# Kernel optimization log

Hardware: AMD Instinct MI355X
Metric: run time of the kernel (lower is better)

## Reference

```python
import jax, jax.numpy as jnp
from jax import lax
import numpy as np

B, L, E, D, A, M, V, T = 64, 196, 2048, 512, 512, 512, 30000, 21


def setup_inputs() -> dict:
    key = jax.random.key(0)
    ks = jax.random.split(key, 22)
    s = 0.02
    encoder_out = jax.random.normal(ks[0], (B, L, E), jnp.float32)
    captions = jax.random.randint(ks[1], (B, T), 0, V, dtype=jnp.int32)
    lens = jax.random.randint(ks[2], (B,), 2, T + 1, dtype=jnp.int32)
    caption_lengths = jnp.sort(lens)[::-1]  # descending, as torch loop requires
    p = {
        'W_enc': jax.random.normal(ks[3], (E, A)) * s, 'b_enc': jnp.zeros((A,)),
        'W_dec': jax.random.normal(ks[4], (D, A)) * s, 'b_dec': jnp.zeros((A,)),
        'w_att': jax.random.normal(ks[5], (A, 1)) * s, 'b_att': jnp.zeros((1,)),
        'emb': jax.random.uniform(ks[6], (V, M), minval=-0.1, maxval=0.1),
        'W_ih': jax.random.normal(ks[7], (M + E, 4 * D)) * s, 'b_ih': jnp.zeros((4 * D,)),
        'W_hh': jax.random.normal(ks[8], (D, 4 * D)) * s, 'b_hh': jnp.zeros((4 * D,)),
        'W_h0': jax.random.normal(ks[9], (E, D)) * s, 'b_h0': jnp.zeros((D,)),
        'W_c0': jax.random.normal(ks[10], (E, D)) * s, 'b_c0': jnp.zeros((D,)),
        'W_beta': jax.random.normal(ks[11], (D, E)) * s, 'b_beta': jnp.zeros((E,)),
        'W_fc': jax.random.uniform(ks[12], (D, V), minval=-0.1, maxval=0.1), 'b_fc': jnp.zeros((V,)),
    }
    return {'encoder_out': encoder_out, 'captions': captions,
            'caption_lengths': caption_lengths, **p}


def reference(encoder_out, captions, caption_lengths,
              W_enc, b_enc, W_dec, b_dec, w_att, b_att, emb,
              W_ih, b_ih, W_hh, b_hh, W_h0, b_h0, W_c0, b_c0,
              W_beta, b_beta, W_fc, b_fc):
    max_len = captions.shape[1] - 1  # teacher forcing: predict y_1..y_T
    x_emb = emb[captions]            # [B,T,M]  (dropout = identity in eval)

    mean_enc = encoder_out.mean(axis=1)
    h0 = jnp.tanh(mean_enc @ W_h0 + b_h0)
    c0 = jnp.tanh(mean_enc @ W_c0 + b_c0)

    # enc projection is constant across timesteps -> hoist out of the loop
    e_proj = encoder_out @ W_enc + b_enc  # [B,L,A]

    # mask[b,t] = (caption_lengths[b]-1) > t  (valid only because lens sorted desc,
    # matching the torch batch_t truncation exactly)
    mask = (caption_lengths[:, None] - 1) > jnp.arange(max_len)[None, :]

    def step(carry, xs):
        h, c = carry
        emb_t, m = xs  # [B,M], [B]
        d = h @ W_dec + b_dec                                   # [B,A]
        energy = (jax.nn.relu(e_proj + d[:, None, :]) @ w_att)[..., 0] + b_att[0]  # [B,L]
        alpha = jax.nn.softmax(energy, axis=1)
        ctx = jnp.einsum('ble,bl->be', encoder_out, alpha)      # [B,E]
        gate = jax.nn.sigmoid(h @ W_beta + b_beta)
        x = jnp.concatenate([emb_t, gate * ctx], axis=1)        # [B,M+E]
        gates = x @ W_ih + b_ih + h @ W_hh + b_hh               # [B,4D]
        i, f, g, o = jnp.split(gates, 4, axis=1)
        c_new = jax.nn.sigmoid(f) * c + jax.nn.sigmoid(i) * jnp.tanh(g)
        h_new = jax.nn.sigmoid(o) * jnp.tanh(c_new)
        pred = h_new @ W_fc + b_fc                              # [B,V]
        mf = m[:, None].astype(pred.dtype)
        return (h_new, c_new), (pred * mf, alpha * mf)

    xs = (jnp.swapaxes(x_emb[:, :max_len, :], 0, 1), mask.T)    # time-major
    _, (preds, alphas) = lax.scan(step, (h0, c0), xs)
    predictions = jnp.swapaxes(preds, 0, 1)                     # [B,max_len,V]
    alphas = jnp.swapaxes(alphas, 0, 1)                         # [B,max_len,L]
    return predictions, alphas
```

## Files before the change

kernel.cpp:

```cpp
#include <hip/hip_runtime.h>
#include <math.h>

namespace {

constexpr int NB  = 64;
constexpr int NL  = 196;
constexpr int NE  = 2048;
constexpr int ND  = 512;
constexpr int NA  = 512;
constexpr int NM  = 512;
constexpr int NV  = 30000;
constexpr int NT  = 21;
constexpr int NML = 20;
constexpr int NG  = 4 * ND;
constexpr int KXG = NM + NE;
constexpr int KSPL = 8, KSL = KXG / KSPL;
constexpr int NDG = ND + NE + NG;
constexpr int OFF_GATE = ND;
constexpr int OFF_HWHH = ND + NE;

constexpr size_t WS_MEAN = 0;
constexpr size_t WS_C0   = WS_MEAN + (size_t)NB * NE;
constexpr size_t WS_C1   = WS_C0   + (size_t)NB * ND;
constexpr size_t WS_D    = WS_C1   + (size_t)NB * ND;
constexpr size_t WS_GATE = WS_D    + (size_t)NB * NA;
constexpr size_t WS_HWHH = WS_GATE + (size_t)NB * NE;
constexpr size_t WS_EN   = WS_HWHH + (size_t)NB * NG;
constexpr size_t WS_PP   = WS_EN   + (size_t)NB * NL;
constexpr size_t WS_SHB  = WS_PP   + (size_t)1048576;
constexpr size_t SH_HALL = 0;
constexpr size_t SH_XEMB = SH_HALL + (size_t)(NML + 1) * NB * ND;
constexpr size_t SH_GCTX = SH_XEMB + (size_t)NML * NB * NM;
constexpr size_t SH_EPROJ= SH_GCTX + (size_t)NB * NE;
constexpr size_t SH_WET  = SH_EPROJ+ (size_t)NB * NL * NA;
constexpr size_t SH_WIHX = SH_WET  + (size_t)NA * NE;
constexpr size_t SH_WALL = SH_WIHX + (size_t)NG * KXG;
constexpr size_t SH_WFC  = SH_WALL + (size_t)NDG * ND;
constexpr size_t SH_ENCBF= SH_WFC  + (size_t)NV * ND;
constexpr size_t SH_END  = SH_ENCBF+ (size_t)NB * NL * NE;
constexpr size_t BYTES_ENC = WS_SHB * 4 + SH_END * 2;

typedef __attribute__((ext_vector_type(8))) short short8v;
typedef __attribute__((ext_vector_type(4))) float f32x4;

__device__ __forceinline__ float sigmoidf_(float x) { return 1.f / (1.f + expf(-x)); }
__device__ __forceinline__ short f2bf(float f) {
  unsigned u = __float_as_uint(f);
  return (short)((u + 0x7FFFu + ((u >> 16) & 1u)) >> 16);
}
__device__ __forceinline__ float bf2f(short s) {
  return __uint_as_float(((unsigned)(unsigned short)s) << 16);
}


__device__ __forceinline__ void gload16(const short* g, short* l) {
  __builtin_amdgcn_global_load_lds(
      (const __attribute__((address_space(1))) unsigned int*)(g),
      (__attribute__((address_space(3))) unsigned int*)(l), 16, 0, 0);
}

template <int R>
__device__ __forceinline__ void stage_direct(const short* __restrict__ src, int ldK,
                                             int rowClamp, short* lds, int tid) {
  int wv = tid >> 6, lane = tid & 63;
  int sub = lane >> 3;
  int kb  = (lane & 7) ^ sub;
#pragma unroll
  for (int g = wv; g < R / 8; g += 4) {
    int row = g * 8 + sub;
    int r = row < rowClamp ? row : rowClamp;
    gload16(src + (size_t)r * ldK + (kb << 3), lds + g * 512);
  }
}

template <int R>
__device__ __forceinline__ void stage_f32cvt(const float* __restrict__ src, int ldK,
                                             short* lds, int tid) {
#pragma unroll
  for (int cidx = tid; cidx < R * 8; cidx += 256) {
    int row = cidx >> 3, kb = cidx & 7;
    const float* p = src + (size_t)row * ldK + kb * 8;
    float4 x = *(const float4*)p;
    float4 y = *(const float4*)(p + 4);
    short8v s;
    s[0] = f2bf(x.x); s[1] = f2bf(x.y); s[2] = f2bf(x.z); s[3] = f2bf(x.w);
    s[4] = f2bf(y.x); s[5] = f2bf(y.y); s[6] = f2bf(y.z); s[7] = f2bf(y.w);
    *(short8v*)(lds + row * 64 + ((kb ^ (row & 7)) << 3)) = s;
  }
}

template <int FM, int FN>
__device__ __forceinline__ void mma_tiles(const short* ldsA, const short* ldsB,
                                          int wr, int wc, int lane, f32x4 acc[FM][FN]) {
  int l15 = lane & 15;
#pragma unroll
  for (int kk = 0; kk < 2; ++kk) {
    int kb0 = kk * 4 + (lane >> 4);
    short8v a[FM], b[FN];
#pragma unroll
    for (int m = 0; m < FM; ++m) {
      int row = wr * FM * 16 + m * 16 + l15;
      a[m] = *(const short8v*)(ldsA + row * 64 + ((kb0 ^ (row & 7)) << 3));
    }
#pragma unroll
    for (int n = 0; n < FN; ++n) {
      int row = wc * FN * 16 + n * 16 + l15;
      b[n] = *(const short8v*)(ldsB + row * 64 + ((kb0 ^ (row & 7)) << 3));
    }
#pragma unroll
    for (int m = 0; m < FM; ++m)
#pragma unroll
      for (int n = 0; n < FN; ++n)
        acc[m][n] = __builtin_amdgcn_mfma_f32_16x16x32_bf16(a[m], b[n], acc[m][n], 0, 0, 0);
  }
}


template <bool PERM>
__global__ __launch_bounds__(256) void k_tcvt(const float* __restrict__ src, int Ks, int Ns,
                                              short* __restrict__ dst, int ldDst, int kOff) {
  __shared__ float tbuf[32][33];
  int n0 = blockIdx.x * 32, k0 = blockIdx.y * 32;
  int tx = threadIdx.x, ty = threadIdx.y;
#pragma unroll
  for (int i = 0; i < 32; i += 8) {
    int k = k0 + ty + i, n = n0 + tx;
    tbuf[ty + i][tx] = (k < Ks && n < Ns) ? src[(size_t)k * Ns + n] : 0.f;
  }
  __syncthreads();
#pragma unroll
  for (int i = 0; i < 32; i += 8) {
    int n = n0 + ty + i, k = k0 + tx;
    if (n < Ns && k < Ks) {
      int nd = PERM ? (((n & 511) << 2) | (n >> 9)) : n;
      dst[(size_t)nd * ldDst + kOff + k] = f2bf(tbuf[tx][ty + i]);
    }
  }
}

template <bool BF>
__global__ __launch_bounds__(256) void k_prep(const float* __restrict__ enc,
                                              short* __restrict__ encbf,
                                              float* __restrict__ mean_enc) {
  int b = blockIdx.y;
  int e = blockIdx.x * 256 + threadIdx.x;
  const float* p = enc + (size_t)b * NL * NE + e;
  short* q = encbf + (size_t)b * NL * NE + e;
  float s = 0.f;
  for (int l = 0; l < NL; ++l) {
    float v = p[(size_t)l * NE];
    s += v;
    if (BF) q[(size_t)l * NE] = f2bf(v);
  }
  mean_enc[(size_t)b * NE + e] = s * (1.f / NL);
}

__global__ void k_xemb(const int* __restrict__ caps, const float* __restrict__ emb,
                       short* __restrict__ xemb) {
  int i = blockIdx.x * 256 + threadIdx.x;
  int m = i & (NM - 1), b = (i >> 9) & (NB - 1), t = i >> 15;
  xemb[i] = f2bf(emb[(size_t)caps[b * NT + t] * NM + m]);
}

__global__ void k_init0(const float* __restrict__ mean_enc, const float* __restrict__ W_h0,
                        const float* __restrict__ W_c0, float* __restrict__ PP) {
  int idx = blockIdx.x * 256 + threadIdx.x;
  int ks = blockIdx.y;
  int b = idx >> 10, jh = idx & 1023, half = jh >> 9, j = jh & 511;
  const float* W = half ? W_c0 : W_h0;
  const float* mp = mean_enc + (size_t)b * NE + ks * 128;
  const float* Wp = W + (size_t)(ks * 128) * ND + j;
  float acc = 0.f;
#pragma unroll 4
  for (int k = 0; k < 128; ++k) acc = fmaf(mp[k], Wp[(size_t)k * ND], acc);
  PP[(size_t)ks * 65536 + idx] = acc;
}

__global__ void k_init1(const float* __restrict__ PP, const float* __restrict__ b_h0,
                        const float* __restrict__ b_c0, float* __restrict__ c0,
                        short* __restrict__ h0) {
  int idx = blockIdx.x * 256 + threadIdx.x;
  int b = idx >> 9, j = idx & 511;
  float ah = b_h0[j], ac = b_c0[j];
  for (int s = 0; s < 16; ++s) {
    const float* p = PP + (size_t)s * 65536 + b * 1024;
    ah += p[j]; ac += p[512 + j];
  }
  c0[idx] = tanhf(ac);
  h0[idx] = f2bf(tanhf(ah));
}

template <bool BF>
__global__ __launch_bounds__(256) void k_eproj(const float* __restrict__ enc,
                                               const short* __restrict__ encbf,
                                               const short* __restrict__ We_t,
                                               const float* __restrict__ b_enc,
                                               short* __restrict__ e_proj) {
  constexpr int FM = 4, FN = 4;
  __shared__ short ldsA[128 * 64], ldsB[128 * 64];
  int p = blockIdx.x;
  int l = (p & 7) * 49 + (p >> 3);
  int bn = (l & 3) * 128, bm = (l >> 2) * 128;
  int tid = threadIdx.x, lane = tid & 63, wave = tid >> 6, wr = wave >> 1, wc = wave & 1;
  f32x4 acc[FM][FN];
#pragma unroll
  for (int m = 0; m < FM; ++m)
#pragma unroll
    for (int n = 0; n < FN; ++n) acc[m][n] = (f32x4){0.f, 0.f, 0.f, 0.f};
  for (int k0 = 0; k0 < NE; k0 += 64) {
    __syncthreads();
    if (BF) stage_direct<128>(encbf + (size_t)bm * NE + k0, NE, 127, ldsA, tid);
    else    stage_f32cvt<128>(enc + (size_t)bm * NE + k0, NE, ldsA, tid);
    stage_direct<128>(We_t + (size_t)bn * NE + k0, NE, 127, ldsB, tid);
    __syncthreads();
    mma_tiles<FM, FN>(ldsA, ldsB, wr, wc, lane, acc);
  }
#pragma unroll
  for (int m = 0; m < FM; ++m)
#pragma unroll
    for (int n = 0; n < FN; ++n) {
      int col = bn + wc * FN * 16 + n * 16 + (lane & 15);
      float bias = b_enc[col];
#pragma unroll
      for (int r = 0; r < 4; ++r) {
        int row = bm + wr * FM * 16 + m * 16 + (lane >> 4) * 4 + r;
        e_proj[(size_t)row * NA + col] = f2bf(acc[m][n][r] + bias);
      }
    }
}

__global__ __launch_bounds__(256) void k_hgemm_dg(const short* __restrict__ h_bf,
                                                  const short* __restrict__ Wall_t,
                                                  const float* __restrict__ b_dec,
                                                  const float* __restrict__ b_beta,
                                                  float* __restrict__ d_buf,
                                                  float* __restrict__ gatebuf,
                                                  float* __restrict__ hWhh) {
  constexpr int FM = 2, FN = 2;
  __shared__ short ldsA[64 * 64], ldsB[64 * 64];
  int bn = blockIdx.x * 64;
  int tid = threadIdx.x, lane = tid & 63, wave = tid >> 6, wr = wave >> 1, wc = wave & 1;
  f32x4 acc[FM][FN];
#pragma unroll
  for (int m = 0; m < FM; ++m)
#pragma unroll
    for (int n = 0; n < FN; ++n) acc[m][n] = (f32x4){0.f, 0.f, 0.f, 0.f};
  for (int k0 = 0; k0 < ND; k0 += 64) {
    __syncthreads();
    stage_direct<64>(h_bf + k0, ND, 63, ldsA, tid);
    stage_direct<64>(Wall_t + (size_t)bn * ND + k0, ND, 63, ldsB, tid);
    __syncthreads();
    mma_tiles<FM, FN>(ldsA, ldsB, wr, wc, lane, acc);
  }
#pragma unroll
  for (int m = 0; m < FM; ++m)
#pragma unroll
    for (int r = 0; r < 4; ++r) {
      int row = wr * FM * 16 + m * 16 + (lane >> 4) * 4 + r;
#pragma unroll
      for (int n = 0; n < FN; ++n) {
        int col = bn + wc * FN * 16 + n * 16 + (lane & 15);
        float a = acc[m][n][r];
        if (bn < OFF_GATE) {
          d_buf[(size_t)row * NA + col] = a + b_dec[col];
        } else if (bn < OFF_HWHH) {
          int e = col - OFF_GATE;
          gatebuf[(size_t)row * NE + e] = sigmoidf_(a + b_beta[e]);
        } else {
          hWhh[(size_t)row * NG + (col - OFF_HWHH)] = a;
        }
      }
    }
}


__global__ __launch_bounds__(256) void k_energy(const short* __restrict__ e_proj,
                                                const float* __restrict__ d_buf,
                                                const float* __restrict__ w_att,
                                                const float* __restrict__ b_att,
                                                float* __restrict__ energy) {
  int tid = threadIdx.x, wave = tid >> 6, lane = tid & 63;
  int row = blockIdx.x * 4 + wave;
  int b = row / NL;
  short8v ev = *(const short8v*)(e_proj + (size_t)row * NA + lane * 8);
  const float* dp = d_buf + (size_t)b * NA + lane * 8;
  float4 d0 = *(const float4*)dp, d1 = *(const float4*)(dp + 4);
  const float* wp = w_att + lane * 8;
  float4 w0 = *(const float4*)wp, w1 = *(const float4*)(wp + 4);
  float dd[8] = {d0.x, d0.y, d0.z, d0.w, d1.x, d1.y, d1.z, d1.w};
  float ww[8] = {w0.x, w0.y, w0.z, w0.w, w1.x, w1.y, w1.z, w1.w};
  float acc = 0.f;
#pragma unroll
  for (int i = 0; i < 8; ++i) {
    float v = bf2f(ev[i]) + dd[i];
    acc = fmaf(fmaxf(v, 0.f), ww[i], acc);
  }
#pragma unroll
  for (int off = 32; off; off >>= 1) acc += __shfl_down(acc, off);
  if (lane == 0) energy[row] = acc + b_att[0];
}

template <bool BF>
__global__ __launch_bounds__(256) void k_ctx(const short* __restrict__ encbf,
                                             const float* __restrict__ encf,
                                             const float* __restrict__ energy,
                                             const float* __restrict__ gatebuf,
                                             const int* __restrict__ clen,
                                             short* __restrict__ gctx,
                                             float* __restrict__ alphas_out, int t) {
  int b = blockIdx.y, e0 = blockIdx.x * 512, tid = threadIdx.x;
  __shared__ float al[NL];
  __shared__ float red[8];
  int wave = tid >> 6, lane = tid & 63;
  float v = (tid < NL) ? energy[b * NL + tid] : -INFINITY;
  float mx = v;
#pragma unroll
  for (int off = 32; off; off >>= 1) mx = fmaxf(mx, __shfl_down(mx, off));
  if (lane == 0) red[wave] = mx;
  __syncthreads();
  if (tid == 0) red[0] = fmaxf(fmaxf(red[0], red[1]), fmaxf(red[2], red[3]));
  __syncthreads();
  mx = red[0];
  float ex = (tid < NL) ? expf(v - mx) : 0.f;
  float sm = ex;
#pragma unroll
  for (int off = 32; off; off >>= 1) sm += __shfl_down(sm, off);
  if (lane == 0) red[4 + wave] = sm;
  __syncthreads();
  if (tid == 0) red[0] = 1.f / (red[4] + red[5] + red[6] + red[7]);
  __syncthreads();
  float alv = ex * red[0];
  if (tid < NL) {
    al[tid] = alv;
    if (blockIdx.x == 0) {
      float mf = ((clen[b] - 1) > t) ? 1.f : 0.f;
      alphas_out[((size_t)b * NML + t) * NL + tid] = alv * mf;
    }
  }
  __syncthreads();
  float cx0 = 0.f, cx1 = 0.f;
  if (BF) {
    const unsigned* p = (const unsigned*)(encbf + (size_t)b * NL * NE + e0) + tid;
#pragma unroll 4
    for (int l = 0; l < NL; ++l) {
      unsigned u = p[(size_t)l * (NE / 2)];
      cx0 = fmaf(al[l], bf2f((short)(u & 0xffffu)), cx0);
      cx1 = fmaf(al[l], bf2f((short)(u >> 16)), cx1);
    }
  } else {
    const float* p = encf + (size_t)b * NL * NE + e0 + 2 * tid;
#pragma unroll 4
    for (int l = 0; l < NL; ++l) {
      float2 u = *(const float2*)(p + (size_t)l * NE);
      cx0 = fmaf(al[l], u.x, cx0);
      cx1 = fmaf(al[l], u.y, cx1);
    }
  }
  int e = e0 + 2 * tid;
  const float* gp = gatebuf + (size_t)b * NE + e;
  unsigned out = (unsigned)(unsigned short)f2bf(cx0 * gp[0]) |
                 ((unsigned)(unsigned short)f2bf(cx1 * gp[1]) << 16);
  *(unsigned*)(gctx + (size_t)b * NE + e) = out;
}

__global__ __launch_bounds__(256) void k_gates(const short* __restrict__ xemb_t,
                                               const short* __restrict__ gctx,
                                               const short* __restrict__ Wihx_t,
                                               float* __restrict__ P) {
  constexpr int FM = 2, FN = 2;
  __shared__ short ldsA[64 * 64], ldsB[64 * 64];
  int bn = blockIdx.x * 64, ks = blockIdx.y;
  int tid = threadIdx.x, lane = tid & 63, wave = tid >> 6, wr = wave >> 1, wc = wave & 1;
  f32x4 acc[FM][FN];
#pragma unroll
  for (int m = 0; m < FM; ++m)
#pragma unroll
    for (int n = 0; n < FN; ++n) acc[m][n] = (f32x4){0.f, 0.f, 0.f, 0.f};
  int kend = (ks + 1) * KSL;
  for (int k0 = ks * KSL; k0 < kend; k0 += 64) {
    const short* asrc; int aldk;
    if (k0 < NM) { asrc = xemb_t + k0;      aldk = NM; }
    else         { asrc = gctx + (k0 - NM); aldk = NE; }
    __syncthreads();
    stage_direct<64>(asrc, aldk, 63, ldsA, tid);
    stage_direct<64>(Wihx_t + (size_t)bn * KXG + k0, KXG, 63, ldsB, tid);
    __syncthreads();
    mma_tiles<FM, FN>(ldsA, ldsB, wr, wc, lane, acc);
  }
#pragma unroll
  for (int m = 0; m < FM; ++m)
#pragma unroll
    for (int n = 0; n < FN; ++n) {
      int col = bn + wc * FN * 16 + n * 16 + (lane & 15);
#pragma unroll
      for (int r = 0; r < 4; ++r) {
        int row = wr * FM * 16 + m * 16 + (lane >> 4) * 4 + r;
        P[((size_t)ks * NB + row) * NG + col] = acc[m][n][r];
      }
    }
}

__global__ void k_lstm(const float* __restrict__ P, const float* __restrict__ hWhh,
                       const float* __restrict__ b_ih, const float* __restrict__ b_hh,
                       const float* __restrict__ c_prev, float* __restrict__ c_next,
                       short* __restrict__ h_next) {
  int idx = blockIdx.x * 256 + threadIdx.x;
  int b = idx >> 9, j = idx & (ND - 1);
  float4 hw = *(const float4*)&hWhh[(size_t)b * NG + j * 4];
  float gi = b_ih[j] + b_hh[j] + hw.x;
  float gf = b_ih[j + ND] + b_hh[j + ND] + hw.y;
  float gg = b_ih[j + 2 * ND] + b_hh[j + 2 * ND] + hw.z;
  float go = b_ih[j + 3 * ND] + b_hh[j + 3 * ND] + hw.w;
#pragma unroll
  for (int s = 0; s < KSPL; ++s) {
    float4 v = *(const float4*)&P[((size_t)s * NB + b) * NG + j * 4];
    gi += v.x; gf += v.y; gg += v.z; go += v.w;
  }
  float cn = sigmoidf_(gf) * c_prev[idx] + sigmoidf_(gi) * tanhf(gg);
  float hn = sigmoidf_(go) * tanhf(cn);
  c_next[idx] = cn;
  h_next[idx] = f2bf(hn);
}

__global__ __launch_bounds__(256) void k_pred(const short* __restrict__ h_all1,
                                              const short* __restrict__ Wfc_t,
                                              const float* __restrict__ b_fc,
                                              const int* __restrict__ clen,
                                              float* __restrict__ preds) {
  constexpr int FM = 4, FN = 4;
  constexpr int NT_M = 10, NT_N = (NV + 127) / 128;
  constexpr int TOT = NT_M * NT_N;
  __shared__ short ldsA[128 * 64], ldsB[128 * 64];
  int p = blockIdx.x;
  int q = TOT / 8, r8 = TOT % 8;
  int xcd = p & 7, i = p >> 3;
  int l = (xcd < r8 ? xcd * (q + 1) : r8 * (q + 1) + (xcd - r8) * q) + i;
  int bm = (l % NT_M) * 128, bn = (l / NT_M) * 128;
  int tid = threadIdx.x, lane = tid & 63, wave = tid >> 6, wr = wave >> 1, wc = wave & 1;
  int rowClampB = NV - 1 - bn; if (rowClampB > 127) rowClampB = 127;
  f32x4 acc[FM][FN];
#pragma unroll
  for (int m = 0; m < FM; ++m)
#pragma unroll
    for (int n = 0; n < FN; ++n) acc[m][n] = (f32x4){0.f, 0.f, 0.f, 0.f};
  for (int k0 = 0; k0 < ND; k0 += 64) {
    __syncthreads();
    stage_direct<128>(h_all1 + (size_t)bm * ND + k0, ND, 127, ldsA, tid);
    stage_direct<128>(Wfc_t + (size_t)bn * ND + k0, ND, rowClampB, ldsB, tid);
    __syncthreads();
    mma_tiles<FM, FN>(ldsA, ldsB, wr, wc, lane, acc);
  }
#pragma unroll
  for (int m = 0; m < FM; ++m)
#pragma unroll
    for (int n = 0; n < FN; ++n) {
      int col = bn + wc * FN * 16 + n * 16 + (lane & 15);
      if (col < NV) {
        float bias = b_fc[col];
#pragma unroll
        for (int r = 0; r < 4; ++r) {
          int row = bm + wr * FM * 16 + m * 16 + (lane >> 4) * 4 + r;
          int t = row >> 6, b = row & 63;
          float mf = ((clen[b] - 1) > t) ? 1.f : 0.f;
          preds[((size_t)b * NML + t) * NV + col] = mf * (acc[m][n][r] + bias);
        }
      }
    }
}

}

extern "C" void kernel_launch(void* const* d_in, const int* in_sizes, int n_in,
                              void* d_out, int out_size, void* d_ws, size_t ws_size,
                              hipStream_t stream) {
  (void)in_sizes; (void)n_in; (void)out_size;
  const float* enc    = (const float*)d_in[0];
  const int*   caps   = (const int*)d_in[1];
  const int*   clen   = (const int*)d_in[2];
  const float* W_enc  = (const float*)d_in[3];
  const float* b_enc  = (const float*)d_in[4];
  const float* W_dec  = (const float*)d_in[5];
  const float* b_dec  = (const float*)d_in[6];
  const float* w_att  = (const float*)d_in[7];
  const float* b_att  = (const float*)d_in[8];
  const float* emb    = (const float*)d_in[9];
  const float* W_ih   = (const float*)d_in[10];
  const float* b_ih   = (const float*)d_in[11];
  const float* W_hh   = (const float*)d_in[12];
  const float* b_hh   = (const float*)d_in[13];
  const float* W_h0   = (const float*)d_in[14];
  const float* b_h0   = (const float*)d_in[15];
  const float* W_c0   = (const float*)d_in[16];
  const float* b_c0   = (const float*)d_in[17];
  const float* W_beta = (const float*)d_in[18];
  const float* b_beta = (const float*)d_in[19];
  const float* W_fc   = (const float*)d_in[20];
  const float* b_fc   = (const float*)d_in[21];

  float* ws     = (float*)d_ws;
  float* preds  = (float*)d_out;
  float* alphas = preds + (size_t)NB * NML * NV;

  float* mean_enc = ws + WS_MEAN;
  float* cbuf[2]  = {ws + WS_C0, ws + WS_C1};
  float* d_buf    = ws + WS_D;
  float* gatebuf  = ws + WS_GATE;
  float* hWhh     = ws + WS_HWHH;
  float* energy   = ws + WS_EN;
  float* PP       = ws + WS_PP;
  short* shb      = (short*)(ws + WS_SHB);
  short* h_all    = shb + SH_HALL;
  short* xemb     = shb + SH_XEMB;
  short* gctx     = shb + SH_GCTX;
  short* e_proj   = shb + SH_EPROJ;
  short* We_t     = shb + SH_WET;
  short* Wihx_t   = shb + SH_WIHX;
  short* Wall_t   = shb + SH_WALL;
  short* Wfc_t    = shb + SH_WFC;
  short* encbf    = shb + SH_ENCBF;
  const bool use_bf = ws_size >= BYTES_ENC;

  k_tcvt<false><<<dim3(NA / 32, NE / 32), dim3(32, 8), 0, stream>>>(W_enc, NE, NA, We_t, NE, 0);
  k_tcvt<true><<<dim3(NG / 32, KXG / 32), dim3(32, 8), 0, stream>>>(
      W_ih, KXG, NG, Wihx_t, KXG, 0);
  k_tcvt<false><<<dim3(NA / 32, ND / 32), dim3(32, 8), 0, stream>>>(W_dec, ND, NA, Wall_t, ND, 0);
  k_tcvt<false><<<dim3(NE / 32, ND / 32), dim3(32, 8), 0, stream>>>(
      W_beta, ND, NE, Wall_t + (size_t)OFF_GATE * ND, ND, 0);
  k_tcvt<true><<<dim3(NG / 32, ND / 32), dim3(32, 8), 0, stream>>>(
      W_hh, ND, NG, Wall_t + (size_t)OFF_HWHH * ND, ND, 0);
  k_tcvt<false><<<dim3((NV + 31) / 32, ND / 32), dim3(32, 8), 0, stream>>>(
      W_fc, ND, NV, Wfc_t, ND, 0);
  if (use_bf)
    k_prep<true><<<dim3(NE / 256, NB), 256, 0, stream>>>(enc, encbf, mean_enc);
  else
    k_prep<false><<<dim3(NE / 256, NB), 256, 0, stream>>>(enc, encbf, mean_enc);
  k_xemb<<<(NML * NB * NM) / 256, 256, 0, stream>>>(caps, emb, xemb);

  k_init0<<<dim3(256, 16), 256, 0, stream>>>(mean_enc, W_h0, W_c0, PP);
  k_init1<<<(NB * ND) / 256, 256, 0, stream>>>(PP, b_h0, b_c0, cbuf[0], h_all);
  if (use_bf)
    k_eproj<true><<<392, 256, 0, stream>>>(enc, encbf, We_t, b_enc, e_proj);
  else
    k_eproj<false><<<392, 256, 0, stream>>>(enc, encbf, We_t, b_enc, e_proj);
  k_hgemm_dg<<<NDG / 64, 256, 0, stream>>>(h_all, Wall_t, b_dec, b_beta,
                                           d_buf, gatebuf, hWhh);

  for (int t = 0; t < NML; ++t) {
    short* h_next = h_all + (size_t)(t + 1) * NB * ND;
    float* c_prev = cbuf[t & 1];
    float* c_next = cbuf[1 - (t & 1)];
    k_energy<<<(NB * NL) / 4, 256, 0, stream>>>(e_proj, d_buf, w_att, b_att, energy);
    if (use_bf)
      k_ctx<true><<<dim3(NE / 512, NB), 256, 0, stream>>>(encbf, enc, energy, gatebuf,
                                                          clen, gctx, alphas, t);
    else
      k_ctx<false><<<dim3(NE / 512, NB), 256, 0, stream>>>(encbf, enc, energy, gatebuf,
                                                           clen, gctx, alphas, t);
    k_gates<<<dim3(NG / 64, KSPL), 256, 0, stream>>>(xemb + (size_t)t * NB * NM, gctx,
                                                     Wihx_t, PP);
    k_lstm<<<(NB * ND) / 256, 256, 0, stream>>>(PP, hWhh, b_ih, b_hh, c_prev, c_next,
                                                h_next);
    if (t + 1 < NML)
      k_hgemm_dg<<<NDG / 64, 256, 0, stream>>>(h_next, Wall_t, b_dec, b_beta,
                                               d_buf, gatebuf, hWhh);
  }
  k_pred<<<10 * ((NV + 127) / 128), 256, 0, stream>>>(h_all + (size_t)NB * ND, Wfc_t,
                                                      b_fc, clen, preds);
}
```

Baseline: 1.173 ms.

## Fuse attention energy into context kernel and stage prediction stores through LDS

Removes the separate per-step energy kernel. Each context block now computes its batch row's 196 attention energies into shared memory before the softmax, which drops 20 launches and the global round trip for the energies. Because the grid has four E-chunk blocks per batch row, the energy work is done four times over. The prediction GEMM epilogue now writes its accumulators to padded LDS and stores coalesced float4 rows, replacing scattered scalar stores into the large prediction output.

```diff
diff --git a/kernel.cpp b/kernel.cpp
--- a/kernel.cpp
+++ b/kernel.cpp
@@ -274,45 +274,43 @@
 }
 
 
-__global__ __launch_bounds__(256) void k_energy(const short* __restrict__ e_proj,
-                                                const float* __restrict__ d_buf,
-                                                const float* __restrict__ w_att,
-                                                const float* __restrict__ b_att,
-                                                float* __restrict__ energy) {
-  int tid = threadIdx.x, wave = tid >> 6, lane = tid & 63;
-  int row = blockIdx.x * 4 + wave;
-  int b = row / NL;
-  short8v ev = *(const short8v*)(e_proj + (size_t)row * NA + lane * 8);
-  const float* dp = d_buf + (size_t)b * NA + lane * 8;
-  float4 d0 = *(const float4*)dp, d1 = *(const float4*)(dp + 4);
-  const float* wp = w_att + lane * 8;
-  float4 w0 = *(const float4*)wp, w1 = *(const float4*)(wp + 4);
-  float dd[8] = {d0.x, d0.y, d0.z, d0.w, d1.x, d1.y, d1.z, d1.w};
-  float ww[8] = {w0.x, w0.y, w0.z, w0.w, w1.x, w1.y, w1.z, w1.w};
-  float acc = 0.f;
-#pragma unroll
-  for (int i = 0; i < 8; ++i) {
-    float v = bf2f(ev[i]) + dd[i];
-    acc = fmaf(fmaxf(v, 0.f), ww[i], acc);
-  }
-#pragma unroll
-  for (int off = 32; off; off >>= 1) acc += __shfl_down(acc, off);
-  if (lane == 0) energy[row] = acc + b_att[0];
-}
-
 template <bool BF>
-__global__ __launch_bounds__(256) void k_ctx(const short* __restrict__ encbf,
-                                             const float* __restrict__ encf,
-                                             const float* __restrict__ energy,
-                                             const float* __restrict__ gatebuf,
-                                             const int* __restrict__ clen,
-                                             short* __restrict__ gctx,
-                                             float* __restrict__ alphas_out, int t) {
+__global__ __launch_bounds__(256) void k_actx(const short* __restrict__ e_proj,
+                                              const float* __restrict__ d_buf,
+                                              const float* __restrict__ w_att,
+                                              const float* __restrict__ b_att,
+                                              const short* __restrict__ encbf,
+                                              const float* __restrict__ encf,
+                                              const float* __restrict__ gatebuf,
+                                              const int* __restrict__ clen,
+                                              short* __restrict__ gctx,
+                                              float* __restrict__ alphas_out, int t) {
   int b = blockIdx.y, e0 = blockIdx.x * 512, tid = threadIdx.x;
+  __shared__ float e_sh[NL];
   __shared__ float al[NL];
   __shared__ float red[8];
   int wave = tid >> 6, lane = tid & 63;
-  float v = (tid < NL) ? energy[b * NL + tid] : -INFINITY;
+  const float* dp = d_buf + (size_t)b * NA + lane * 8;
+  float4 d0v = *(const float4*)dp, d1v = *(const float4*)(dp + 4);
+  const float* wp = w_att + lane * 8;
+  float4 w0v = *(const float4*)wp, w1v = *(const float4*)(wp + 4);
+  float dd[8] = {d0v.x, d0v.y, d0v.z, d0v.w, d1v.x, d1v.y, d1v.z, d1v.w};
+  float ww[8] = {w0v.x, w0v.y, w0v.z, w0v.w, w1v.x, w1v.y, w1v.z, w1v.w};
+  float batt = b_att[0];
+  for (int l = wave; l < NL; l += 4) {
+    short8v ev = *(const short8v*)(e_proj + (size_t)(b * NL + l) * NA + lane * 8);
+    float acc = 0.f;
+#pragma unroll
+    for (int i = 0; i < 8; ++i) {
+      float v = bf2f(ev[i]) + dd[i];
+      acc = fmaf(fmaxf(v, 0.f), ww[i], acc);
+    }
+#pragma unroll
+    for (int off = 32; off; off >>= 1) acc += __shfl_down(acc, off);
+    if (lane == 0) e_sh[l] = acc + batt;
+  }
+  __syncthreads();
+  float v = (tid < NL) ? e_sh[tid] : -INFINITY;
   float mx = v;
 #pragma unroll
   for (int off = 32; off; off >>= 1) mx = fmaxf(mx, __shfl_down(mx, off));
@@ -430,7 +428,10 @@
   constexpr int FM = 4, FN = 4;
   constexpr int NT_M = 10, NT_N = (NV + 127) / 128;
   constexpr int TOT = NT_M * NT_N;
-  __shared__ short ldsA[128 * 64], ldsB[128 * 64];
+  __shared__ __align__(16) char smem[64 * 129 * 4];
+  short* ldsA = (short*)smem;
+  short* ldsB = ldsA + 128 * 64;
+  float* fl   = (float*)smem;
   int p = blockIdx.x;
   int q = TOT / 8, r8 = TOT % 8;
   int xcd = p & 7, i = p >> 3;
@@ -450,22 +451,44 @@
     __syncthreads();
     mma_tiles<FM, FN>(ldsA, ldsB, wr, wc, lane, acc);
   }
-#pragma unroll
-  for (int m = 0; m < FM; ++m)
-#pragma unroll
-    for (int n = 0; n < FN; ++n) {
-      int col = bn + wc * FN * 16 + n * 16 + (lane & 15);
-      if (col < NV) {
-        float bias = b_fc[col];
-#pragma unroll
-        for (int r = 0; r < 4; ++r) {
-          int row = bm + wr * FM * 16 + m * 16 + (lane >> 4) * 4 + r;
-          int t = row >> 6, b = row & 63;
-          float mf = ((clen[b] - 1) > t) ? 1.f : 0.f;
-          preds[((size_t)b * NML + t) * NV + col] = mf * (acc[m][n][r] + bias);
+  __syncthreads();
+#pragma unroll
+  for (int h = 0; h < 2; ++h) {
+    if (wr == h) {
+#pragma unroll
+      for (int m = 0; m < FM; ++m)
+#pragma unroll
+        for (int n = 0; n < FN; ++n)
+#pragma unroll
+          for (int r = 0; r < 4; ++r) {
+            int lr = m * 16 + (lane >> 4) * 4 + r;
+            int lc = wc * 64 + n * 16 + (lane & 15);
+            fl[lr * 129 + lc] = acc[m][n][r];
+          }
+    }
+    __syncthreads();
+    {
+      int lr = tid & 63, cs = (tid >> 6) * 32;
+      int grow = bm + h * 64 + lr;
+      int tt = grow >> 6, bb = grow & 63;
+      float mf = ((clen[bb] - 1) > tt) ? 1.f : 0.f;
+      size_t obase = ((size_t)bb * NML + tt) * NV + bn + cs;
+#pragma unroll
+      for (int j = 0; j < 8; ++j) {
+        int col = bn + cs + j * 4;
+        if (col < NV) {
+          const float* fp = &fl[lr * 129 + cs + j * 4];
+          float4 v;
+          v.x = mf * (fp[0] + b_fc[col]);
+          v.y = mf * (fp[1] + b_fc[col + 1]);
+          v.z = mf * (fp[2] + b_fc[col + 2]);
+          v.w = mf * (fp[3] + b_fc[col + 3]);
+          *(float4*)(preds + obase + j * 4) = v;
         }
       }
     }
+    __syncthreads();
+  }
 }
 
 }
@@ -506,7 +529,6 @@
   float* d_buf    = ws + WS_D;
   float* gatebuf  = ws + WS_GATE;
   float* hWhh     = ws + WS_HWHH;
-  float* energy   = ws + WS_EN;
   float* PP       = ws + WS_PP;
   short* shb      = (short*)(ws + WS_SHB);
   short* h_all    = shb + SH_HALL;
@@ -549,13 +571,14 @@
     short* h_next = h_all + (size_t)(t + 1) * NB * ND;
     float* c_prev = cbuf[t & 1];
     float* c_next = cbuf[1 - (t & 1)];
-    k_energy<<<(NB * NL) / 4, 256, 0, stream>>>(e_proj, d_buf, w_att, b_att, energy);
     if (use_bf)
-      k_ctx<true><<<dim3(NE / 512, NB), 256, 0, stream>>>(encbf, enc, energy, gatebuf,
-                                                          clen, gctx, alphas, t);
+      k_actx<true><<<dim3(NE / 512, NB), 256, 0, stream>>>(e_proj, d_buf, w_att, b_att,
+                                                           encbf, enc, gatebuf, clen,
+                                                           gctx, alphas, t);
     else
-      k_ctx<false><<<dim3(NE / 512, NB), 256, 0, stream>>>(encbf, enc, energy, gatebuf,
-                                                           clen, gctx, alphas, t);
+      k_actx<false><<<dim3(NE / 512, NB), 256, 0, stream>>>(e_proj, d_buf, w_att, b_att,
+                                                            encbf, enc, gatebuf, clen,
+                                                            gctx, alphas, t);
     k_gates<<<dim3(NG / 64, KSPL), 256, 0, stream>>>(xemb + (size_t)t * NB * NM, gctx,
                                                      Wihx_t, PP);
     k_lstm<<<(NB * ND) / 256, 256, 0, stream>>>(PP, hWhh, b_ih, b_hh, c_prev, c_next,
```

Measured after the change: 1.655 ms. +41.1%, slower.
